# Kernel optimization log

Hardware: AMD Instinct MI355X
Metric: run time of the kernel (lower is better)

## Reference

```python
import jax, jax.numpy as jnp
import numpy as np

HEADS = 4
DIM_HEAD = 32
CHUNK = 1024
GROUPS = 8
EPS = 1e-5


def setup_inputs() -> dict:
    key = jax.random.key(0)
    k1, k2, k3 = jax.random.split(key, 3)
    b, dim, h, w = 8, 64, 96, 96
    inner = HEADS * DIM_HEAD  # 128
    x = jax.random.normal(k1, (b, dim, h, w), dtype=jnp.float32)
    W_qkv = jax.random.normal(k2, (3 * inner, dim), dtype=jnp.float32) * (1.0 / np.sqrt(dim))
    W_out = jax.random.normal(k3, (dim, inner), dtype=jnp.float32) * (1.0 / np.sqrt(inner))
    b_out = jnp.zeros((dim,), dtype=jnp.float32)
    gamma = jnp.ones((dim,), dtype=jnp.float32)
    beta = jnp.zeros((dim,), dtype=jnp.float32)
    return {"x": x, "W_qkv": W_qkv, "W_out": W_out, "b_out": b_out,
            "gamma": gamma, "beta": beta}


def reference(x, W_qkv, W_out, b_out, gamma, beta):
    b, c, h, w = x.shape
    n = h * w
    nch = n // CHUNK  # number of full chunks (n chosen divisible by CHUNK)
    d = DIM_HEAD
    BH = b * HEADS

    # 1x1 conv (no bias) == matmul over channel dim
    xf = x.reshape(b, c, n)
    qkv = jnp.einsum('oc,bcn->bon', W_qkv, xf)          # [b, 3*inner, n]
    q, k, v = jnp.split(qkv, 3, axis=1)                  # each [b, inner, n]

    def chunkify(t):
        # [b, inner, n] -> [BH, nch, d, CHUNK]; slicing i:i+CHUNK on last axis
        # equals reshaping n -> (nch, CHUNK) in order.
        return t.reshape(BH, d, nch, CHUNK).transpose(0, 2, 1, 3)

    qc, kc, vc = chunkify(q), chunkify(k), chunkify(v)

    qs = jax.nn.softmax(qc, axis=-1)  # softmax over chunk spatial positions
    ks = jax.nn.softmax(kc, axis=-2)  # softmax over head channels

    # context = k_chunk^T @ v_chunk : [BH, nch, CHUNK, CHUNK]
    ctx = jnp.einsum('gkdi,gkdj->gkij', ks, vc)
    # chunk_out = q_chunk @ context : [BH, nch, d, CHUNK]
    out = jnp.einsum('gkdi,gkij->gkdj', qs, ctx)

    # concat chunks back along spatial dim, reshape to image layout
    out = out.transpose(0, 2, 1, 3).reshape(b, HEADS * d, h, w)

    # to_out: 1x1 conv with bias, then GroupNorm(8, dim)
    y = jnp.einsum('oc,bchw->bohw', W_out, out) + b_out[None, :, None, None]

    yg = y.reshape(b, GROUPS, c // GROUPS, h, w)
    mu = jnp.mean(yg, axis=(2, 3, 4), keepdims=True)
    var = jnp.var(yg, axis=(2, 3, 4), keepdims=True)
    yn = ((yg - mu) * jax.lax.rsqrt(var + EPS)).reshape(b, c, h, w)
    return yn * gamma[None, :, None, None] + beta[None, :, None, None]
```

## Files before the change

### kernel.cpp

```cpp
#include <hip/hip_runtime.h>
#include <hip/hip_bf16.h>

#define N_POS 9216
#define NCHUNK 9
#define BATCH 8
#define CDIM 64
#define HEADS 4
#define EPS 1e-5f

#define VSEC_SZ ((size_t)BATCH * N_POS * 128)
#define VSEC_BYTES (VSEC_SZ * 2)
#define PPART_SZ ((size_t)32 * NCHUNK * 1024)
#define NPART 16
#define UBF_BYTES ((size_t)BATCH * NCHUNK * 64 * 128 * 2)

typedef __attribute__((ext_vector_type(8))) short short8;
typedef __attribute__((ext_vector_type(4))) float f32x4;

static __device__ inline unsigned pk2(float a, float b) {
    __hip_bfloat162 h2(__float2bfloat16(a), __float2bfloat16(b));
    return *reinterpret_cast<unsigned*>(&h2);
}
static __device__ inline float bf2f(short s) {
    union { unsigned u; float f; } c; c.u = ((unsigned)(unsigned short)s) << 16; return c.f;
}

__global__ __launch_bounds__(256) void wprep_kernel(const float* __restrict__ Wqkv,
        __hip_bfloat16* __restrict__ wbf) {
    int i = blockIdx.x * 256 + threadIdx.x;
    if (i < 6144) {
        float4 v = ((const float4*)Wqkv)[i];
        uint2 u; u.x = pk2(v.x, v.y); u.y = pk2(v.z, v.w);
        ((uint2*)wbf)[i] = u;
    }
}

__global__ __launch_bounds__(256) void qkp_kernel(const float* __restrict__ x,
        const __hip_bfloat16* __restrict__ wbf, float* __restrict__ Pparts) {
    int bx = blockIdx.x;
    int b  = blockIdx.y;
    int ck = bx >> 4, pt = bx & 15;
    int n0 = bx * 64;
    __shared__ __align__(16) char lraw[36864];
    __hip_bfloat16 (*xs)[72]  = (__hip_bfloat16(*)[72])lraw;
    __hip_bfloat16 (*skT)[72] = (__hip_bfloat16(*)[72])lraw;
    int t = threadIdx.x, w = t >> 6, l = t & 63;
    int l15 = l & 15, quad = l >> 4;

    {
        int p = t & 63, cbase = (t >> 6) * 16;
        const float* xb = x + (size_t)b * CDIM * N_POS + n0 + p;
        #pragma unroll
        for (int j = 0; j < 16; j += 4) {
            float v0 = xb[(size_t)(cbase + j + 0) * N_POS];
            float v1 = xb[(size_t)(cbase + j + 1) * N_POS];
            float v2 = xb[(size_t)(cbase + j + 2) * N_POS];
            float v3 = xb[(size_t)(cbase + j + 3) * N_POS];
            uint2 u; u.x = pk2(v0, v1); u.y = pk2(v2, v3);
            *reinterpret_cast<uint2*>(&xs[p][cbase + j]) = u;
        }
    }
    __syncthreads();

    f32x4 acc[4][4];
    #pragma unroll
    for (int mt = 0; mt < 4; ++mt)
        #pragma unroll
        for (int nt = 0; nt < 4; ++nt) acc[mt][nt] = (f32x4){0.f, 0.f, 0.f, 0.f};
    #pragma unroll
    for (int ks = 0; ks < 2; ++ks) {
        int k0 = ks * 32 + quad * 8;
        short8 av[4];
        #pragma unroll
        for (int mt = 0; mt < 4; ++mt)
            av[mt] = *reinterpret_cast<const short8*>(&xs[mt * 16 + l15][k0]);
        #pragma unroll
        for (int nt = 0; nt < 4; ++nt) {
            short8 bw = *reinterpret_cast<const short8*>(wbf + (size_t)(w * 64 + nt * 16 + l15) * 64 + k0);
            #pragma unroll
            for (int mt = 0; mt < 4; ++mt)
                acc[mt][nt] = __builtin_amdgcn_mfma_f32_16x16x32_bf16(av[mt], bw, acc[mt][nt], 0, 0, 0);
        }
    }
    __syncthreads();

    #pragma unroll
    for (int nt = 0; nt < 4; ++nt) {
        int ch = w * 64 + nt * 16 + l15;
        #pragma unroll
        for (int mt = 0; mt < 4; ++mt) {
            uint2 u;
            u.x = pk2(acc[mt][nt][0], acc[mt][nt][1]);
            u.y = pk2(acc[mt][nt][2], acc[mt][nt][3]);
            *reinterpret_cast<uint2*>(&skT[ch][mt * 16 + quad * 4]) = u;
        }
    }
    __syncthreads();

    {
        int p = t & 63, h = t >> 6;
        float kr[32]; float mx = -1e30f;
        #pragma unroll
        for (int d = 0; d < 32; ++d) { kr[d] = bf2f(*(const short*)&skT[128 + h * 32 + d][p]); mx = fmaxf(mx, kr[d]); }
        float s = 0.f;
        #pragma unroll
        for (int d = 0; d < 32; ++d) { kr[d] = __expf(kr[d] - mx); s += kr[d]; }
        float is = 1.f / s;
        #pragma unroll
        for (int d = 0; d < 32; ++d) skT[128 + h * 32 + d][p] = __float2bfloat16(kr[d] * is);
        #pragma unroll
        for (int d = 0; d < 32; ++d) {
            float qv = bf2f(*(const short*)&skT[h * 32 + d][p]);
            skT[h * 32 + d][p] = __float2bfloat16(__expf(qv));
        }
    }
    __syncthreads();

    f32x4 pac[2][2];
    pac[0][0] = (f32x4){0,0,0,0}; pac[0][1] = (f32x4){0,0,0,0};
    pac[1][0] = (f32x4){0,0,0,0}; pac[1][1] = (f32x4){0,0,0,0};
    #pragma unroll
    for (int step = 0; step < 2; ++step) {
        int k0 = step * 32 + quad * 8;
        short8 bk[2];
        #pragma unroll
        for (int nt = 0; nt < 2; ++nt)
            bk[nt] = *reinterpret_cast<const short8*>(&skT[128 + w * 32 + nt * 16 + l15][k0]);
        #pragma unroll
        for (int mt = 0; mt < 2; ++mt) {
            short8 aq = *reinterpret_cast<const short8*>(&skT[w * 32 + mt * 16 + l15][k0]);
            pac[mt][0] = __builtin_amdgcn_mfma_f32_16x16x32_bf16(aq, bk[0], pac[mt][0], 0, 0, 0);
            pac[mt][1] = __builtin_amdgcn_mfma_f32_16x16x32_bf16(aq, bk[1], pac[mt][1], 0, 0, 0);
        }
    }
    float* Pp = Pparts + (size_t)pt * PPART_SZ + ((size_t)(b * 4 + w) * NCHUNK + ck) * 1024;
    #pragma unroll
    for (int mt = 0; mt < 2; ++mt)
        #pragma unroll
        for (int nt = 0; nt < 2; ++nt)
            #pragma unroll
            for (int r = 0; r < 4; ++r)
                Pp[(mt * 16 + quad * 4 + r) * 32 + nt * 16 + l15] = pac[mt][nt][r];
}

__global__ __launch_bounds__(256) void v_kernel(const float* __restrict__ x,
        const __hip_bfloat16* __restrict__ wbf, __hip_bfloat16* __restrict__ vsec) {
    int n0 = blockIdx.x * 128;
    int b  = blockIdx.y;
    __shared__ __align__(16) char lraw[34816];
    __hip_bfloat16 (*xs)[72]    = (__hip_bfloat16(*)[72])lraw;
    __hip_bfloat16 (*vbuf)[136] = (__hip_bfloat16(*)[136])lraw;
    int t = threadIdx.x, w = t >> 6, l = t & 63;
    int l15 = l & 15, quad = l >> 4;

    {
        int p = t & 127, cbase = (t >> 7) * 32;
        const float* xb = x + (size_t)b * CDIM * N_POS + n0 + p;
        #pragma unroll
        for (int j = 0; j < 32; j += 4) {
            float v0 = xb[(size_t)(cbase + j + 0) * N_POS];
            float v1 = xb[(size_t)(cbase + j + 1) * N_POS];
            float v2 = xb[(size_t)(cbase + j + 2) * N_POS];
            float v3 = xb[(size_t)(cbase + j + 3) * N_POS];
            uint2 u; u.x = pk2(v0, v1); u.y = pk2(v2, v3);
            *reinterpret_cast<uint2*>(&xs[p][cbase + j]) = u;
        }
    }
    __syncthreads();

    int nw = w * 32;
    f32x4 acc[8][2];
    #pragma unroll
    for (int mt = 0; mt < 8; ++mt) { acc[mt][0] = (f32x4){0,0,0,0}; acc[mt][1] = (f32x4){0,0,0,0}; }
    #pragma unroll
    for (int ks = 0; ks < 2; ++ks) {
        int k0 = ks * 32 + quad * 8;
        short8 bfr[2];
        #pragma unroll
        for (int nt = 0; nt < 2; ++nt)
            bfr[nt] = *reinterpret_cast<const short8*>(&xs[nw + nt * 16 + l15][k0]);
        #pragma unroll
        for (int mt = 0; mt < 8; ++mt) {
            short8 afr = *reinterpret_cast<const short8*>(wbf + (size_t)(256 + mt * 16 + l15) * 64 + k0);
            acc[mt][0] = __builtin_amdgcn_mfma_f32_16x16x32_bf16(afr, bfr[0], acc[mt][0], 0, 0, 0);
            acc[mt][1] = __builtin_amdgcn_mfma_f32_16x16x32_bf16(afr, bfr[1], acc[mt][1], 0, 0, 0);
        }
    }
    __syncthreads();

    #pragma unroll
    for (int mt = 0; mt < 8; ++mt)
        #pragma unroll
        for (int nt = 0; nt < 2; ++nt) {
            int p = nw + nt * 16 + l15;
            uint2 u;
            u.x = pk2(acc[mt][nt][0], acc[mt][nt][1]);
            u.y = pk2(acc[mt][nt][2], acc[mt][nt][3]);
            *reinterpret_cast<uint2*>(&vbuf[p][mt * 16 + quad * 4]) = u;
        }
    __syncthreads();

    __hip_bfloat16* outb = vsec + ((size_t)b * N_POS + n0) * 128;
    int rg = t >> 4, c0 = (t & 15) * 8;
    #pragma unroll
    for (int j = 0; j < 8; ++j) {
        int r = j * 16 + rg;
        *reinterpret_cast<uint4*>(outb + (size_t)r * 128 + c0) =
            *reinterpret_cast<const uint4*>(&vbuf[r][c0]);
    }
}

__global__ __launch_bounds__(256) void umat_kernel(const float* __restrict__ Wout,
        const float* __restrict__ Pparts, __hip_bfloat16* __restrict__ Ubf,
        float* __restrict__ stats) {
    int ck = blockIdx.x, b = blockIdx.y, h = blockIdx.z;
    int bh = b * 4 + h;
    int t = threadIdx.x;
    if (ck == 0 && h == 0 && t < 16) stats[b * 16 + t] = 0.f;
    __shared__ float Pl[32][32];
    __shared__ float iZ[32];
    size_t base4 = ((size_t)bh * NCHUNK + ck) * 256;
    {
        const float4* P0 = (const float4*)Pparts + base4 + t;
        float4 s = (float4){0.f, 0.f, 0.f, 0.f};
        #pragma unroll
        for (int j = 0; j < NPART; ++j) {
            float4 a = P0[j * (PPART_SZ / 4)];
            s.x += a.x; s.y += a.y; s.z += a.z; s.w += a.w;
        }
        ((float4*)Pl)[t] = s;
    }
    __syncthreads();
    if (t < 32) {
        float s = 0.f;
        #pragma unroll
        for (int c = 0; c < 32; ++c) s += Pl[t][c];
        iZ[t] = 1.f / s;
    }
    __syncthreads();
    int o = t & 63, wv = t >> 6;
    float wz[32];
    {
        const float4* wr = (const float4*)(Wout + (size_t)o * 128 + h * 32);
        #pragma unroll
        for (int j = 0; j < 8; ++j) {
            float4 f = wr[j];
            wz[j*4+0] = f.x * iZ[j*4+0]; wz[j*4+1] = f.y * iZ[j*4+1];
            wz[j*4+2] = f.z * iZ[j*4+2]; wz[j*4+3] = f.w * iZ[j*4+3];
        }
    }
    float ua[8];
    #pragma unroll
    for (int j = 0; j < 8; ++j) ua[j] = 0.f;
    for (int d = 0; d < 32; ++d) {
        float wd = wz[d];
        #pragma unroll
        for (int j = 0; j < 8; ++j) ua[j] += wd * Pl[d][wv * 8 + j];
    }
    uint4 up;
    up.x = pk2(ua[0], ua[1]); up.y = pk2(ua[2], ua[3]);
    up.z = pk2(ua[4], ua[5]); up.w = pk2(ua[6], ua[7]);
    __hip_bfloat16* Up = Ubf + ((size_t)(b * NCHUNK + ck) * 64 + o) * 128 + h * 32 + wv * 8;
    *reinterpret_cast<uint4*>(Up) = up;
}

__global__ __launch_bounds__(256) void y_kernel(const __hip_bfloat16* __restrict__ vsec,
        const __hip_bfloat16* __restrict__ Ubf, const float* __restrict__ bout,
        float* __restrict__ y, float* __restrict__ stats) {
    int bx = blockIdx.x;
    int b  = blockIdx.y;
    int ck = bx >> 3;
    __shared__ float gsum[8], gsq[8];
    int t = threadIdx.x, w = t >> 6, l = t & 63;
    int l15 = l & 15, quad = l >> 4;
    if (t < 8) { gsum[t] = 0.f; gsq[t] = 0.f; }
    __syncthreads();
    const __hip_bfloat16* vt = vsec + (size_t)b * N_POS * 128;
    const __hip_bfloat16* Ub = Ubf + (size_t)(b * NCHUNK + ck) * 64 * 128;
    int nbase = bx * 128 + w * 32;
    f32x4 acc[4][2];
    #pragma unroll
    for (int mt = 0; mt < 4; ++mt) { acc[mt][0] = (f32x4){0,0,0,0}; acc[mt][1] = (f32x4){0,0,0,0}; }
    #pragma unroll
    for (int ks = 0; ks < 4; ++ks) {
        int k0 = ks * 32 + quad * 8;
        short8 bf[2];
        #pragma unroll
        for (int nt = 0; nt < 2; ++nt)
            bf[nt] = *reinterpret_cast<const short8*>(vt + (size_t)(nbase + nt * 16 + l15) * 128 + k0);
        #pragma unroll
        for (int mt = 0; mt < 4; ++mt) {
            short8 af = *reinterpret_cast<const short8*>(Ub + (size_t)(mt * 16 + l15) * 128 + k0);
            acc[mt][0] = __builtin_amdgcn_mfma_f32_16x16x32_bf16(af, bf[0], acc[mt][0], 0, 0, 0);
            acc[mt][1] = __builtin_amdgcn_mfma_f32_16x16x32_bf16(af, bf[1], acc[mt][1], 0, 0, 0);
        }
    }
    float gsl[4], gql[4];
    #pragma unroll
    for (int mt = 0; mt < 4; ++mt) { gsl[mt] = 0.f; gql[mt] = 0.f; }
    float* yb = y + (size_t)b * CDIM * N_POS;
    #pragma unroll
    for (int mt = 0; mt < 4; ++mt) {
        float4 bo = *reinterpret_cast<const float4*>(bout + mt * 16 + quad * 4);
        const float* bop = reinterpret_cast<const float*>(&bo);
        #pragma unroll
        for (int nt = 0; nt < 2; ++nt) {
            int n = nbase + nt * 16 + l15;
            #pragma unroll
            for (int r = 0; r < 4; ++r) {
                int o = mt * 16 + quad * 4 + r;
                float val = acc[mt][nt][r] + bop[r];
                yb[(size_t)o * N_POS + n] = val;
                gsl[mt] += val; gql[mt] += val * val;
            }
        }
    }
    #pragma unroll
    for (int off = 16; off >= 1; off >>= 1) {
        #pragma unroll
        for (int mt = 0; mt < 4; ++mt) {
            gsl[mt] += __shfl_xor(gsl[mt], off, 64);
            gql[mt] += __shfl_xor(gql[mt], off, 64);
        }
    }
    if (l == 0 || l == 32) {
        int qh = quad >> 1;
        #pragma unroll
        for (int mt = 0; mt < 4; ++mt) {
            atomicAdd(&gsum[2 * mt + qh], gsl[mt]);
            atomicAdd(&gsq[2 * mt + qh], gql[mt]);
        }
    }
    __syncthreads();
    if (t < 8) {
        atomicAdd(&stats[(b * 8 + t) * 2],     gsum[t]);
        atomicAdd(&stats[(b * 8 + t) * 2 + 1], gsq[t]);
    }
}

__global__ __launch_bounds__(256) void gn_kernel(float* __restrict__ y,
        const float* __restrict__ stats, const float* __restrict__ gamma,
        const float* __restrict__ beta) {
    int i4 = blockIdx.x * 256 + threadIdx.x;
    if (i4 >= (BATCH * CDIM * N_POS) / 4) return;
    int base = i4 * 4;
    int bc = base / N_POS;
    int c = bc & 63, b = bc >> 6;
    int g = c >> 3;
    float s = stats[(b * 8 + g) * 2], q = stats[(b * 8 + g) * 2 + 1];
    const float invN = 1.f / (8.f * N_POS);
    float mean = s * invN;
    float var = q * invN - mean * mean;
    float sc = rsqrtf(var + EPS);
    float ga = gamma[c] * sc;
    float be = beta[c] - mean * sc * gamma[c];
    float4 v = ((float4*)y)[i4];
    v.x = v.x * ga + be; v.y = v.y * ga + be; v.z = v.z * ga + be; v.w = v.w * ga + be;
    ((float4*)y)[i4] = v;
}

extern "C" void kernel_launch(void* const* d_in, const int* in_sizes, int n_in,
                              void* d_out, int out_size, void* d_ws, size_t ws_size,
                              hipStream_t stream) {
    const float* x     = (const float*)d_in[0];
    const float* Wqkv  = (const float*)d_in[1];
    const float* Wout  = (const float*)d_in[2];
    const float* bout  = (const float*)d_in[3];
    const float* gamma = (const float*)d_in[4];
    const float* beta  = (const float*)d_in[5];
    float* out = (float*)d_out;

    __hip_bfloat16* vsec = (__hip_bfloat16*)d_ws;
    float* stats  = (float*)((char*)d_ws + VSEC_BYTES);
    float* Pparts = stats + 128;
    __hip_bfloat16* Ubf = (__hip_bfloat16*)(Pparts + NPART * PPART_SZ);
    __hip_bfloat16* wbf = (__hip_bfloat16*)((char*)Ubf + UBF_BYTES);

    wprep_kernel<<<dim3(24), 256, 0, stream>>>(Wqkv, wbf);
    qkp_kernel<<<dim3(144, BATCH), 256, 0, stream>>>(x, wbf, Pparts);
    v_kernel<<<dim3(72, BATCH), 256, 0, stream>>>(x, wbf, vsec);
    umat_kernel<<<dim3(NCHUNK, BATCH, HEADS), 256, 0, stream>>>(Wout, Pparts, Ubf, stats);
    y_kernel<<<dim3(72, BATCH), 256, 0, stream>>>(vsec, Ubf, bout, out, stats);
    gn_kernel<<<dim3((BATCH * CDIM * N_POS / 4 + 255) / 256), 256, 0, stream>>>(out, stats, gamma, beta);
}
```

Baseline: 134.0 us.

## Fuse V projection into y kernel, keeping V tile in shared memory

The separate v_kernel that computed V = Wv·x and wrote it to a bf16 workspace is removed. Its work now runs at the start of the y kernel, with the V tile staged in LDS and read directly by the U·V MFMA. This drops a kernel launch and an 18.9 MB bf16 write plus re-read of V through global memory. In exchange, the fused kernel does more work per block, and V is now computed after umat rather than able to overlap with it.

```diff
diff --git a/kernel.cpp b/kernel.cpp
--- a/kernel.cpp
+++ b/kernel.cpp
@@ -8,8 +8,6 @@
 #define HEADS 4
 #define EPS 1e-5f
 
-#define VSEC_SZ ((size_t)BATCH * N_POS * 128)
-#define VSEC_BYTES (VSEC_SZ * 2)
 #define PPART_SZ ((size_t)32 * NCHUNK * 1024)
 #define NPART 16
 #define UBF_BYTES ((size_t)BATCH * NCHUNK * 64 * 128 * 2)
@@ -143,73 +141,6 @@
                 Pp[(mt * 16 + quad * 4 + r) * 32 + nt * 16 + l15] = pac[mt][nt][r];
 }
 
-__global__ __launch_bounds__(256) void v_kernel(const float* __restrict__ x,
-        const __hip_bfloat16* __restrict__ wbf, __hip_bfloat16* __restrict__ vsec) {
-    int n0 = blockIdx.x * 128;
-    int b  = blockIdx.y;
-    __shared__ __align__(16) char lraw[34816];
-    __hip_bfloat16 (*xs)[72]    = (__hip_bfloat16(*)[72])lraw;
-    __hip_bfloat16 (*vbuf)[136] = (__hip_bfloat16(*)[136])lraw;
-    int t = threadIdx.x, w = t >> 6, l = t & 63;
-    int l15 = l & 15, quad = l >> 4;
-
-    {
-        int p = t & 127, cbase = (t >> 7) * 32;
-        const float* xb = x + (size_t)b * CDIM * N_POS + n0 + p;
-        #pragma unroll
-        for (int j = 0; j < 32; j += 4) {
-            float v0 = xb[(size_t)(cbase + j + 0) * N_POS];
-            float v1 = xb[(size_t)(cbase + j + 1) * N_POS];
-            float v2 = xb[(size_t)(cbase + j + 2) * N_POS];
-            float v3 = xb[(size_t)(cbase + j + 3) * N_POS];
-            uint2 u; u.x = pk2(v0, v1); u.y = pk2(v2, v3);
-            *reinterpret_cast<uint2*>(&xs[p][cbase + j]) = u;
-        }
-    }
-    __syncthreads();
-
-    int nw = w * 32;
-    f32x4 acc[8][2];
-    #pragma unroll
-    for (int mt = 0; mt < 8; ++mt) { acc[mt][0] = (f32x4){0,0,0,0}; acc[mt][1] = (f32x4){0,0,0,0}; }
-    #pragma unroll
-    for (int ks = 0; ks < 2; ++ks) {
-        int k0 = ks * 32 + quad * 8;
-        short8 bfr[2];
-        #pragma unroll
-        for (int nt = 0; nt < 2; ++nt)
-            bfr[nt] = *reinterpret_cast<const short8*>(&xs[nw + nt * 16 + l15][k0]);
-        #pragma unroll
-        for (int mt = 0; mt < 8; ++mt) {
-            short8 afr = *reinterpret_cast<const short8*>(wbf + (size_t)(256 + mt * 16 + l15) * 64 + k0);
-            acc[mt][0] = __builtin_amdgcn_mfma_f32_16x16x32_bf16(afr, bfr[0], acc[mt][0], 0, 0, 0);
-            acc[mt][1] = __builtin_amdgcn_mfma_f32_16x16x32_bf16(afr, bfr[1], acc[mt][1], 0, 0, 0);
-        }
-    }
-    __syncthreads();
-
-    #pragma unroll
-    for (int mt = 0; mt < 8; ++mt)
-        #pragma unroll
-        for (int nt = 0; nt < 2; ++nt) {
-            int p = nw + nt * 16 + l15;
-            uint2 u;
-            u.x = pk2(acc[mt][nt][0], acc[mt][nt][1]);
-            u.y = pk2(acc[mt][nt][2], acc[mt][nt][3]);
-            *reinterpret_cast<uint2*>(&vbuf[p][mt * 16 + quad * 4]) = u;
-        }
-    __syncthreads();
-
-    __hip_bfloat16* outb = vsec + ((size_t)b * N_POS + n0) * 128;
-    int rg = t >> 4, c0 = (t & 15) * 8;
-    #pragma unroll
-    for (int j = 0; j < 8; ++j) {
-        int r = j * 16 + rg;
-        *reinterpret_cast<uint4*>(outb + (size_t)r * 128 + c0) =
-            *reinterpret_cast<const uint4*>(&vbuf[r][c0]);
-    }
-}
-
 __global__ __launch_bounds__(256) void umat_kernel(const float* __restrict__ Wout,
         const float* __restrict__ Pparts, __hip_bfloat16* __restrict__ Ubf,
         float* __restrict__ stats) {
@@ -264,20 +195,71 @@
     *reinterpret_cast<uint4*>(Up) = up;
 }
 
-__global__ __launch_bounds__(256) void y_kernel(const __hip_bfloat16* __restrict__ vsec,
-        const __hip_bfloat16* __restrict__ Ubf, const float* __restrict__ bout,
-        float* __restrict__ y, float* __restrict__ stats) {
+__global__ __launch_bounds__(256) void vy_kernel(const float* __restrict__ x,
+        const __hip_bfloat16* __restrict__ wbf, const __hip_bfloat16* __restrict__ Ubf,
+        const float* __restrict__ bout, float* __restrict__ y, float* __restrict__ stats) {
     int bx = blockIdx.x;
     int b  = blockIdx.y;
     int ck = bx >> 3;
+    int n0 = bx * 128;
+    __shared__ __align__(16) char lraw[34816];
+    __hip_bfloat16 (*xs)[72]    = (__hip_bfloat16(*)[72])lraw;
+    __hip_bfloat16 (*vbuf)[136] = (__hip_bfloat16(*)[136])lraw;
     __shared__ float gsum[8], gsq[8];
     int t = threadIdx.x, w = t >> 6, l = t & 63;
     int l15 = l & 15, quad = l >> 4;
     if (t < 8) { gsum[t] = 0.f; gsq[t] = 0.f; }
-    __syncthreads();
-    const __hip_bfloat16* vt = vsec + (size_t)b * N_POS * 128;
+
+    {
+        int p = t & 127, cbase = (t >> 7) * 32;
+        const float* xb = x + (size_t)b * CDIM * N_POS + n0 + p;
+        #pragma unroll
+        for (int j = 0; j < 32; j += 4) {
+            float v0 = xb[(size_t)(cbase + j + 0) * N_POS];
+            float v1 = xb[(size_t)(cbase + j + 1) * N_POS];
+            float v2 = xb[(size_t)(cbase + j + 2) * N_POS];
+            float v3 = xb[(size_t)(cbase + j + 3) * N_POS];
+            uint2 u; u.x = pk2(v0, v1); u.y = pk2(v2, v3);
+            *reinterpret_cast<uint2*>(&xs[p][cbase + j]) = u;
+        }
+    }
+    __syncthreads();
+
+    int nw = w * 32;
+    {
+        f32x4 vacc[8][2];
+        #pragma unroll
+        for (int mt = 0; mt < 8; ++mt) { vacc[mt][0] = (f32x4){0,0,0,0}; vacc[mt][1] = (f32x4){0,0,0,0}; }
+        #pragma unroll
+        for (int ks = 0; ks < 2; ++ks) {
+            int k0 = ks * 32 + quad * 8;
+            short8 bfr[2];
+            #pragma unroll
+            for (int nt = 0; nt < 2; ++nt)
+                bfr[nt] = *reinterpret_cast<const short8*>(&xs[nw + nt * 16 + l15][k0]);
+            #pragma unroll
+            for (int mt = 0; mt < 8; ++mt) {
+                short8 afr = *reinterpret_cast<const short8*>(wbf + (size_t)(256 + mt * 16 + l15) * 64 + k0);
+                vacc[mt][0] = __builtin_amdgcn_mfma_f32_16x16x32_bf16(afr, bfr[0], vacc[mt][0], 0, 0, 0);
+                vacc[mt][1] = __builtin_amdgcn_mfma_f32_16x16x32_bf16(afr, bfr[1], vacc[mt][1], 0, 0, 0);
+            }
+        }
+        __syncthreads();
+
+        #pragma unroll
+        for (int mt = 0; mt < 8; ++mt)
+            #pragma unroll
+            for (int nt = 0; nt < 2; ++nt) {
+                int p = nw + nt * 16 + l15;
+                uint2 u;
+                u.x = pk2(vacc[mt][nt][0], vacc[mt][nt][1]);
+                u.y = pk2(vacc[mt][nt][2], vacc[mt][nt][3]);
+                *reinterpret_cast<uint2*>(&vbuf[p][mt * 16 + quad * 4]) = u;
+            }
+    }
+    __syncthreads();
+
     const __hip_bfloat16* Ub = Ubf + (size_t)(b * NCHUNK + ck) * 64 * 128;
-    int nbase = bx * 128 + w * 32;
     f32x4 acc[4][2];
     #pragma unroll
     for (int mt = 0; mt < 4; ++mt) { acc[mt][0] = (f32x4){0,0,0,0}; acc[mt][1] = (f32x4){0,0,0,0}; }
@@ -287,7 +269,7 @@
         short8 bf[2];
         #pragma unroll
         for (int nt = 0; nt < 2; ++nt)
-            bf[nt] = *reinterpret_cast<const short8*>(vt + (size_t)(nbase + nt * 16 + l15) * 128 + k0);
+            bf[nt] = *reinterpret_cast<const short8*>(&vbuf[nw + nt * 16 + l15][k0]);
         #pragma unroll
         for (int mt = 0; mt < 4; ++mt) {
             short8 af = *reinterpret_cast<const short8*>(Ub + (size_t)(mt * 16 + l15) * 128 + k0);
@@ -299,6 +281,7 @@
     #pragma unroll
     for (int mt = 0; mt < 4; ++mt) { gsl[mt] = 0.f; gql[mt] = 0.f; }
     float* yb = y + (size_t)b * CDIM * N_POS;
+    int nbase = n0 + nw;
     #pragma unroll
     for (int mt = 0; mt < 4; ++mt) {
         float4 bo = *reinterpret_cast<const float4*>(bout + mt * 16 + quad * 4);
@@ -370,16 +353,14 @@
     const float* beta  = (const float*)d_in[5];
     float* out = (float*)d_out;
 
-    __hip_bfloat16* vsec = (__hip_bfloat16*)d_ws;
-    float* stats  = (float*)((char*)d_ws + VSEC_BYTES);
+    float* stats  = (float*)d_ws;
     float* Pparts = stats + 128;
     __hip_bfloat16* Ubf = (__hip_bfloat16*)(Pparts + NPART * PPART_SZ);
     __hip_bfloat16* wbf = (__hip_bfloat16*)((char*)Ubf + UBF_BYTES);
 
     wprep_kernel<<<dim3(24), 256, 0, stream>>>(Wqkv, wbf);
     qkp_kernel<<<dim3(144, BATCH), 256, 0, stream>>>(x, wbf, Pparts);
-    v_kernel<<<dim3(72, BATCH), 256, 0, stream>>>(x, wbf, vsec);
     umat_kernel<<<dim3(NCHUNK, BATCH, HEADS), 256, 0, stream>>>(Wout, Pparts, Ubf, stats);
-    y_kernel<<<dim3(72, BATCH), 256, 0, stream>>>(vsec, Ubf, bout, out, stats);
+    vy_kernel<<<dim3(72, BATCH), 256, 0, stream>>>(x, wbf, Ubf, bout, out, stats);
     gn_kernel<<<dim3((BATCH * CDIM * N_POS / 4 + 255) / 256), 256, 0, stream>>>(out, stats, gamma, beta);
 }
```

New measurement: 126.6 us. 1.06x faster.
